# Kernel optimization log

Hardware: AMD Instinct MI355X
Metric: run time of the kernel (lower is better)

Reference implementation:

```python
import jax, jax.numpy as jnp
import numpy as np

B, N, M = 8192, 4096, 256


def setup_inputs() -> dict:
    key = jax.random.key(0)
    k_x, k_keep, k_w1, k_b1, k_w2, k_b2 = jax.random.split(key, 6)
    x = jax.random.normal(k_x, (B, N), dtype=jnp.float32)
    keep = jax.random.uniform(k_keep, (B, N)) < 0.5
    x = jnp.where(keep, x, 0.0)
    # Linear params, PyTorch-style fan-in scaling
    W1 = jax.random.normal(k_w1, (N, M), dtype=jnp.float32) / np.sqrt(N)
    b1 = jax.random.normal(k_b1, (M,), dtype=jnp.float32) * 0.01
    W2 = jax.random.normal(k_w2, (M, N), dtype=jnp.float32) / np.sqrt(M)
    b2 = jax.random.normal(k_b2, (N,), dtype=jnp.float32) * 0.01
    return {"x": x, "W1": W1, "b1": b1, "W2": W2, "b2": b2}


def reference(x, W1, b1, W2, b2):
    # f2(relu(f1(x)))
    f = jax.nn.relu(x @ W1 + b1) @ W2 + b2  # [B, N]
    mask = x != 0
    # per-row sum over masked positions (vectorized version of the Python loop)
    s = jnp.sum(jnp.where(mask, f, 0.0), axis=1, keepdims=True)  # [B, 1]
    # rows with empty mask stay all-zero; guard divide-by-zero for those rows
    s_safe = jnp.where(s == 0.0, 1.0, s)
    y = jnp.where(mask, f / s_safe, 0.0)
    return y
```

## Files before the change

### kernel.cpp

```cpp
#include <hip/hip_runtime.h>

typedef _Float16 f16;
typedef _Float16 f16x8 __attribute__((ext_vector_type(8)));
typedef float f32x4 __attribute__((ext_vector_type(4)));

#define MFMA16(a,b,c) __builtin_amdgcn_mfma_f32_16x16x32_f16((a),(b),(c),0,0,0)

__device__ __forceinline__ void gload16(const void* g, void* l) {
  __builtin_amdgcn_global_load_lds(
      (const __attribute__((address_space(1))) void*)g,
      (__attribute__((address_space(3))) void*)l, 16, 0, 0);
}

__device__ __forceinline__ int swz(int r, int c) {
  return r * 32 + ((c ^ (r & 3)) << 3);
}

__device__ __forceinline__ void split8n(const f32x4 v0, const f32x4 v1,
                                        f16x8& hv, f16x8& lv) {
#pragma unroll
  for (int j = 0; j < 4; ++j) {
    f16 h0 = (f16)v0[j]; hv[j] = h0; lv[j] = (f16)(v0[j] - (float)h0);
    f16 h1 = (f16)v1[j]; hv[j + 4] = h1; lv[j + 4] = (f16)(v1[j] - (float)h1);
  }
}

__global__ __launch_bounds__(256) void k_prep(const float* __restrict__ in,
                                              f16* __restrict__ oh, f16* __restrict__ ol,
                                              int R, int C, int trShift) {
  __shared__ float t[64][65];
  int c0 = blockIdx.x * 64, r0 = blockIdx.y * 64;
  int tid = threadIdx.x;
#pragma unroll
  for (int i = 0; i < 16; ++i) {
    int idx = tid + i * 256;
    int r = idx >> 6, c = idx & 63;
    t[r][c] = in[(size_t)(r0 + r) * C + (c0 + c)];
  }
  __syncthreads();
  int ktiles = R >> 5;
  int TRm1 = (1 << trShift) - 1;
#pragma unroll
  for (int w = 0; w < 2; ++w) {
    int idx = tid + w * 256;
    int nn = idx >> 3, cc8 = idx & 7;
    f32x4 v0, v1;
#pragma unroll
    for (int j = 0; j < 4; ++j) v0[j] = t[cc8 * 8 + j][nn];
#pragma unroll
    for (int j = 0; j < 4; ++j) v1[j] = t[cc8 * 8 + 4 + j][nn];
    f16x8 hv, lv;
    split8n(v0, v1, hv, lv);
    int gn = c0 + nn, gk = r0 + cc8 * 8;
    size_t tileIdx = (size_t)(gn >> trShift) * ktiles + (gk >> 5);
    size_t off = (tileIdx << (trShift + 5)) + ((size_t)(gn & TRm1) << 5) +
                 (((cc8 & 3) ^ (gn & 3)) << 3);
    *(f16x8*)&oh[off] = hv;
    *(f16x8*)&ol[off] = lv;
  }
}

__global__ __launch_bounds__(256, 2) void k_g1(
    const float* __restrict__ X, const f16* __restrict__ Bht,
    const f16* __restrict__ Blt, unsigned short* __restrict__ mb2,
    float* __restrict__ partials) {
  __shared__ f16 smA[2][2][4096];
  __shared__ f16 smB[2][2][4096];
  int bx = blockIdx.x, nb = blockIdx.y, kc = blockIdx.z;
  int tid = threadIdx.x;
  int wv = tid >> 6, ln = tid & 63, lr = ln & 15, lg = ln >> 4;
  int wr = wv >> 1, wc = wv & 1;
  const int NS = 32;
  int m0 = bx * 128, kb0 = kc * 1024;
  int arow = tid >> 1, akc = tid & 1;
  const float* xp = X + (size_t)(m0 + arow) * 4096 + kb0 + akc * 16;
  size_t bt0 = ((size_t)nb * 128 + (size_t)kc * 32) * 4096;
  bool domask = (nb == 0);
  int wo0 = swz(arow, 2 * akc);
  int wo1 = swz(arow, 2 * akc + 1);

  auto stageB = [&](int s, int buf) {
#pragma unroll
    for (int w = 0; w < 2; ++w) {
      size_t o = (size_t)(w * 4 + wv) * 512 + (size_t)ln * 8;
      gload16(Bht + bt0 + (size_t)s * 4096 + o, &smB[buf][0][(w * 4 + wv) * 512]);
      gload16(Blt + bt0 + (size_t)s * 4096 + o, &smB[buf][1][(w * 4 + wv) * 512]);
    }
  };
  auto commitA = [&](f32x4 a0, f32x4 a1, f32x4 a2, f32x4 a3, int buf, int s) {
    f16x8 h0, l0, h1, l1;
    split8n(a0, a1, h0, l0);
    split8n(a2, a3, h1, l1);
    *(f16x8*)&smA[buf][0][wo0] = h0;
    *(f16x8*)&smA[buf][0][wo1] = h1;
    *(f16x8*)&smA[buf][1][wo0] = l0;
    *(f16x8*)&smA[buf][1][wo1] = l1;
    if (domask) {
      unsigned m = 0;
#pragma unroll
      for (int j = 0; j < 4; ++j) {
        if (a0[j] != 0.f) m |= 1u << j;
        if (a1[j] != 0.f) m |= 1u << (4 + j);
        if (a2[j] != 0.f) m |= 1u << (8 + j);
        if (a3[j] != 0.f) m |= 1u << (12 + j);
      }
      int gk = kb0 + s * 32 + akc * 16;
      mb2[((size_t)(m0 + arow) * 512 + (gk >> 3)) >> 1] = (unsigned short)m;
    }
  };

  f32x4 acc[4][4] = {};

  stageB(0, 0);
  {
    f32x4 a0 = *(const f32x4*)xp, a1 = *(const f32x4*)(xp + 4);
    f32x4 a2 = *(const f32x4*)(xp + 8), a3 = *(const f32x4*)(xp + 12);
    commitA(a0, a1, a2, a3, 0, 0);
  }
  __syncthreads();

  int cur = 0;
  for (int s = 0; s < NS; ++s) {
    f32x4 a0, a1, a2, a3;
    bool more = (s + 1) < NS;
    if (more) {
      const float* xn = xp + (s + 1) * 32;
      a0 = *(const f32x4*)xn; a1 = *(const f32x4*)(xn + 4);
      a2 = *(const f32x4*)(xn + 8); a3 = *(const f32x4*)(xn + 12);
      stageB(s + 1, cur ^ 1);
    }
    f16x8 fah[4], fal[4], fbh[4], fbl[4];
#pragma unroll
    for (int f = 0; f < 4; ++f) {
      int r = wr * 64 + f * 16 + lr;
      fah[f] = *(const f16x8*)&smA[cur][0][swz(r, lg)];
      fal[f] = *(const f16x8*)&smA[cur][1][swz(r, lg)];
      int c = wc * 64 + f * 16 + lr;
      fbh[f] = *(const f16x8*)&smB[cur][0][swz(c, lg)];
      fbl[f] = *(const f16x8*)&smB[cur][1][swz(c, lg)];
    }
#pragma unroll
    for (int fi = 0; fi < 4; ++fi)
#pragma unroll
      for (int fj = 0; fj < 4; ++fj) {
        acc[fi][fj] = MFMA16(fah[fi], fbh[fj], acc[fi][fj]);
        acc[fi][fj] = MFMA16(fah[fi], fbl[fj], acc[fi][fj]);
        acc[fi][fj] = MFMA16(fal[fi], fbh[fj], acc[fi][fj]);
      }
    if (more) commitA(a0, a1, a2, a3, cur ^ 1, s + 1);
    __syncthreads();
    cur ^= 1;
  }

  float* pout = partials + (size_t)kc * 8192 * 256;
#pragma unroll
  for (int fi = 0; fi < 4; ++fi)
#pragma unroll
    for (int fj = 0; fj < 4; ++fj)
#pragma unroll
      for (int q = 0; q < 4; ++q) {
        int row = m0 + wr * 64 + fi * 16 + lg * 4 + q;
        int col = nb * 128 + wc * 64 + fj * 16 + lr;
        pout[(size_t)row * 256 + col] = acc[fi][fj][q];
      }
}

__global__ __launch_bounds__(256) void k_hsplit(const float* __restrict__ p,
                                                const float* __restrict__ b1,
                                                f16* __restrict__ Hh,
                                                f16* __restrict__ Hl) {
  int g = blockIdx.x * 256 + threadIdx.x;
  int r = g >> 5, c = g & 31;
  const size_t CH = (size_t)8192 * 256;
  const float* p0 = p + (size_t)r * 256 + c * 8;
  f32x4 s0 = *(const f32x4*)p0, s1 = *(const f32x4*)(p0 + 4);
#pragma unroll
  for (int q = 1; q < 4; ++q) {
    f32x4 d0 = *(const f32x4*)(p0 + q * CH), d1 = *(const f32x4*)(p0 + q * CH + 4);
#pragma unroll
    for (int j = 0; j < 4; ++j) { s0[j] += d0[j]; s1[j] += d1[j]; }
  }
  f32x4 bb0 = *(const f32x4*)(b1 + c * 8), bb1 = *(const f32x4*)(b1 + c * 8 + 4);
  f32x4 v0, v1;
#pragma unroll
  for (int j = 0; j < 4; ++j) {
    float v = s0[j] + bb0[j];
    v0[j] = v > 0.f ? v : 0.f;
    float w = s1[j] + bb1[j];
    v1[j] = w > 0.f ? w : 0.f;
  }
  f16x8 hv, lv;
  split8n(v0, v1, hv, lv);
  size_t tileIdx = (size_t)(r >> 7) * 8 + (c >> 2);
  size_t off = tileIdx * 4096 + ((size_t)(r & 127) << 5) + (((c & 3) ^ (r & 3)) << 3);
  *(f16x8*)&Hh[off] = hv;
  *(f16x8*)&Hl[off] = lv;
}

__global__ __launch_bounds__(256, 2) void k_gemm2b(
    const f16* __restrict__ At_h, const f16* __restrict__ At_l,
    const f16* __restrict__ Bt_h, const f16* __restrict__ Bt_l,
    const float* __restrict__ b2, const unsigned* __restrict__ maskw,
    f16* __restrict__ fout, float* __restrict__ partials) {
  __shared__ f16 smA[2][2][4096];
  __shared__ f16 smB[2][2][4096];
  __shared__ unsigned mlds[128][4];
  __shared__ float rsum[128][2];
  int bx = blockIdx.x, by = blockIdx.y;
  int m0 = bx * 128, n0 = by * 128;
  int tid = threadIdx.x;
  int wv = tid >> 6, ln = tid & 63, lr = ln & 15, lg = ln >> 4;
  int wr = wv >> 1, wc = wv & 1;
#pragma unroll
  for (int i = 0; i < 2; ++i) {
    int idx = tid + i * 256;
    mlds[idx >> 2][idx & 3] =
        maskw[(size_t)(m0 + (idx >> 2)) * 128 + by * 4 + (idx & 3)];
  }
  size_t at0 = (size_t)bx * 8 * 4096;
  size_t bt0 = (size_t)by * 8 * 4096;

  auto stage = [&](int s, int buf) {
#pragma unroll
    for (int w = 0; w < 2; ++w) {
      size_t o = (size_t)(w * 4 + wv) * 512 + (size_t)ln * 8;
      gload16(At_h + at0 + (size_t)s * 4096 + o, &smA[buf][0][(w * 4 + wv) * 512]);
      gload16(At_l + at0 + (size_t)s * 4096 + o, &smA[buf][1][(w * 4 + wv) * 512]);
      gload16(Bt_h + bt0 + (size_t)s * 4096 + o, &smB[buf][0][(w * 4 + wv) * 512]);
      gload16(Bt_l + bt0 + (size_t)s * 4096 + o, &smB[buf][1][(w * 4 + wv) * 512]);
    }
  };

  f32x4 acc[4][4] = {};
  stage(0, 0);
  __syncthreads();
  int cur = 0;
  for (int s = 0; s < 8; ++s) {
    if (s + 1 < 8) stage(s + 1, cur ^ 1);
    f16x8 fah[4], fal[4], fbh[4], fbl[4];
#pragma unroll
    for (int f = 0; f < 4; ++f) {
      int r = wr * 64 + f * 16 + lr;
      fah[f] = *(const f16x8*)&smA[cur][0][swz(r, lg)];
      fal[f] = *(const f16x8*)&smA[cur][1][swz(r, lg)];
      int c = wc * 64 + f * 16 + lr;
      fbh[f] = *(const f16x8*)&smB[cur][0][swz(c, lg)];
      fbl[f] = *(const f16x8*)&smB[cur][1][swz(c, lg)];
    }
#pragma unroll
    for (int fi = 0; fi < 4; ++fi)
#pragma unroll
      for (int fj = 0; fj < 4; ++fj) {
        acc[fi][fj] = MFMA16(fah[fi], fbh[fj], acc[fi][fj]);
        acc[fi][fj] = MFMA16(fah[fi], fbl[fj], acc[fi][fj]);
        acc[fi][fj] = MFMA16(fal[fi], fbh[fj], acc[fi][fj]);
      }
    __syncthreads();
    cur ^= 1;
  }

  float rp[4][4] = {};
#pragma unroll
  for (int fi = 0; fi < 4; ++fi)
#pragma unroll
    for (int fj = 0; fj < 4; ++fj)
#pragma unroll
      for (int q = 0; q < 4; ++q) {
        int row = wr * 64 + fi * 16 + lg * 4 + q;
        int col = wc * 64 + fj * 16 + lr;
        float v = acc[fi][fj][q] + b2[n0 + col];
        unsigned wd = mlds[row][col >> 5];
        float mv = ((wd >> (col & 31)) & 1u) ? v : 0.f;
        fout[(size_t)(m0 + row) * 4096 + (n0 + col)] = (f16)mv;
        rp[fi][q] += mv;
      }
#pragma unroll
  for (int fi = 0; fi < 4; ++fi)
#pragma unroll
    for (int q = 0; q < 4; ++q) {
      float sv = rp[fi][q];
      sv += __shfl_xor(sv, 1);
      sv += __shfl_xor(sv, 2);
      sv += __shfl_xor(sv, 4);
      sv += __shfl_xor(sv, 8);
      if (lr == 0) rsum[wr * 64 + fi * 16 + lg * 4 + q][wc] = sv;
    }
  __syncthreads();
  if (tid < 128)
    partials[(size_t)(m0 + tid) * 32 + by] = rsum[tid][0] + rsum[tid][1];
}

__global__ __launch_bounds__(256) void k_rowinv(const float* __restrict__ partials,
                                                float* __restrict__ inv) {
  int r = blockIdx.x * 256 + threadIdx.x;
  if (r < 8192) {
    float s = 0.f;
#pragma unroll 4
    for (int i = 0; i < 32; ++i) s += partials[(size_t)r * 32 + i];
    float ss = (s == 0.f) ? 1.f : s;
    inv[r] = 1.f / ss;
  }
}

__global__ __launch_bounds__(256) void k_scale16(const f16* __restrict__ f,
                                                 const float* __restrict__ inv,
                                                 float* __restrict__ out) {
  int v = blockIdx.x * 256 + threadIdx.x;
  float iv = inv[v >> 9];
  f16x8 d = *(const f16x8*)(f + (size_t)v * 8);
  f32x4 o0, o1;
#pragma unroll
  for (int j = 0; j < 4; ++j) {
    o0[j] = (float)d[j] * iv;
    o1[j] = (float)d[4 + j] * iv;
  }
  *(f32x4*)(out + (size_t)v * 8) = o0;
  *(f32x4*)(out + (size_t)v * 8 + 4) = o1;
}

extern "C" void kernel_launch(void* const* d_in, const int* in_sizes, int n_in,
                              void* d_out, int out_size, void* d_ws, size_t ws_size,
                              hipStream_t stream) {
  const float* x  = (const float*)d_in[0];
  const float* W1 = (const float*)d_in[1];
  const float* b1 = (const float*)d_in[2];
  const float* W2 = (const float*)d_in[3];
  const float* b2 = (const float*)d_in[4];
  float* out = (float*)d_out;
  char* ws = (char*)d_ws;

  const size_t MB = (size_t)1 << 20;
  f16* W1t_h = (f16*)(ws + 0 * MB);
  f16* W1t_l = (f16*)(ws + 2 * MB);
  f16* W2t_h = (f16*)(ws + 4 * MB);
  f16* W2t_l = (f16*)(ws + 6 * MB);
  f16* Hh    = (f16*)(ws + 8 * MB);
  f16* Hl    = (f16*)(ws + 12 * MB);
  unsigned char* mb = (unsigned char*)(ws + 16 * MB);
  float* part1 = (float*)(ws + 20 * MB);
  float* part2 = (float*)(ws + 52 * MB);
  float* inv_s = (float*)(ws + 53 * MB);
  f16* fbuf    = (f16*)(ws + 54 * MB);

  k_prep<<<dim3(4, 64), 256, 0, stream>>>(W1, W1t_h, W1t_l, 4096, 256, 7);
  k_prep<<<dim3(64, 4), 256, 0, stream>>>(W2, W2t_h, W2t_l, 256, 4096, 7);
  k_g1<<<dim3(64, 2, 4), 256, 0, stream>>>(x, W1t_h, W1t_l,
                                           (unsigned short*)mb, part1);
  k_hsplit<<<1024, 256, 0, stream>>>(part1, b1, Hh, Hl);
  k_gemm2b<<<dim3(64, 32), 256, 0, stream>>>(Hh, Hl, W2t_h, W2t_l, b2,
                                             (const unsigned*)mb, fbuf, part2);
  k_rowinv<<<32, 256, 0, stream>>>(part2, inv_s);
  k_scale16<<<16384, 256, 0, stream>>>(fbuf, inv_s, out);
}
```

Measured before the change: 215.2 us.

## Restructure first GEMM: register-resident A fragments, triple-buffered B, split-K 8

The first GEMM kernel now loads X directly into registers in MFMA fragment layout and does the fp16 hi/lo split there, so the A tile no longer goes through shared memory. Blocks shrink to 128 threads (2 waves, each covering 64 rows by all 128 columns). B tiles are triple-buffered with explicit vmcnt waits and raw s_barrier calls so the load for stage s+2 overlaps compute on stage s. Split-K goes from 4 to 8, which raises block count; in exchange the partial buffer doubles and the reduction in k_hsplit reads twice as many partials. This is meant to cut LDS traffic and barrier stalls and to improve latency hiding, at the cost of more accumulator registers and extra partial-sum memory traffic.

Measured after the change: 230.4 us. 7.1% more time.

```diff
diff --git a/kernel.cpp b/kernel.cpp
--- a/kernel.cpp
+++ b/kernel.cpp
@@ -60,107 +60,121 @@
   }
 }
 
-__global__ __launch_bounds__(256, 2) void k_g1(
+__global__ __launch_bounds__(128, 2) void k_g1(
     const float* __restrict__ X, const f16* __restrict__ Bht,
-    const f16* __restrict__ Blt, unsigned short* __restrict__ mb2,
+    const f16* __restrict__ Blt, unsigned char* __restrict__ mb,
     float* __restrict__ partials) {
-  __shared__ f16 smA[2][2][4096];
-  __shared__ f16 smB[2][2][4096];
+  __shared__ f16 smB[3][8192];
   int bx = blockIdx.x, nb = blockIdx.y, kc = blockIdx.z;
   int tid = threadIdx.x;
-  int wv = tid >> 6, ln = tid & 63, lr = ln & 15, lg = ln >> 4;
-  int wr = wv >> 1, wc = wv & 1;
-  const int NS = 32;
-  int m0 = bx * 128, kb0 = kc * 1024;
-  int arow = tid >> 1, akc = tid & 1;
-  const float* xp = X + (size_t)(m0 + arow) * 4096 + kb0 + akc * 16;
-  size_t bt0 = ((size_t)nb * 128 + (size_t)kc * 32) * 4096;
+  int wid = tid >> 6, ln = tid & 63, lr = ln & 15, lg = ln >> 4;
+  const int NS = 16;
+  int m0 = bx * 128, kb0 = kc * 512;
+  size_t bt0 = ((size_t)nb * 128 + (size_t)kc * 16) * 4096;
   bool domask = (nb == 0);
-  int wo0 = swz(arow, 2 * akc);
-  int wo1 = swz(arow, 2 * akc + 1);
-
+
+  const float* xb = X + (size_t)(m0 + wid * 64 + lr) * 4096 + kb0 + lg * 8;
+  const size_t XF = (size_t)16 * 4096;
+
+  f32x4 areg[8];
+  f16x8 ah[4], al[4];
+  f32x4 acc[4][8] = {};
+
+  auto issueA = [&](int s) {
+#pragma unroll
+    for (int fi = 0; fi < 4; ++fi) {
+      const float* p = xb + (size_t)fi * XF + s * 32;
+      areg[fi * 2] = *(const f32x4*)p;
+      areg[fi * 2 + 1] = *(const f32x4*)(p + 4);
+    }
+  };
   auto stageB = [&](int s, int buf) {
-#pragma unroll
-    for (int w = 0; w < 2; ++w) {
-      size_t o = (size_t)(w * 4 + wv) * 512 + (size_t)ln * 8;
-      gload16(Bht + bt0 + (size_t)s * 4096 + o, &smB[buf][0][(w * 4 + wv) * 512]);
-      gload16(Blt + bt0 + (size_t)s * 4096 + o, &smB[buf][1][(w * 4 + wv) * 512]);
-    }
+    const f16* bh = Bht + bt0 + (size_t)s * 4096;
+    const f16* bl = Blt + bt0 + (size_t)s * 4096;
+#pragma unroll
+    for (int i = 0; i < 4; ++i)
+      gload16(bh + ((i * 2 + wid) * 512 + ln * 8), &smB[buf][(i * 2 + wid) * 512]);
+#pragma unroll
+    for (int i = 0; i < 4; ++i)
+      gload16(bl + ((i * 2 + wid) * 512 + ln * 8),
+              &smB[buf][4096 + (i * 2 + wid) * 512]);
   };
-  auto commitA = [&](f32x4 a0, f32x4 a1, f32x4 a2, f32x4 a3, int buf, int s) {
-    f16x8 h0, l0, h1, l1;
-    split8n(a0, a1, h0, l0);
-    split8n(a2, a3, h1, l1);
-    *(f16x8*)&smA[buf][0][wo0] = h0;
-    *(f16x8*)&smA[buf][0][wo1] = h1;
-    *(f16x8*)&smA[buf][1][wo0] = l0;
-    *(f16x8*)&smA[buf][1][wo1] = l1;
+  auto splitA = [&](int s) {
+#pragma unroll
+    for (int fi = 0; fi < 4; ++fi)
+      split8n(areg[fi * 2], areg[fi * 2 + 1], ah[fi], al[fi]);
     if (domask) {
-      unsigned m = 0;
+#pragma unroll
+      for (int fi = 0; fi < 4; ++fi) {
+        unsigned m = 0;
+#pragma unroll
+        for (int j = 0; j < 4; ++j) {
+          if (areg[fi * 2][j] != 0.f) m |= 1u << j;
+          if (areg[fi * 2 + 1][j] != 0.f) m |= 1u << (4 + j);
+        }
+        int row = m0 + wid * 64 + fi * 16 + lr;
+        int gk = kb0 + s * 32 + lg * 8;
+        mb[(size_t)row * 512 + (gk >> 3)] = (unsigned char)m;
+      }
+    }
+  };
+
+  issueA(0);
+  stageB(0, 0);
+  stageB(1, 1);
+  asm volatile("s_waitcnt vmcnt(8)" ::: "memory");
+  __builtin_amdgcn_sched_barrier(0);
+  splitA(0);
+  __builtin_amdgcn_s_barrier();
+
+  int cb = 0;
+  for (int s = 0; s < NS; ++s) {
+    bool moreA = (s + 1) < NS;
+    bool moreB = (s + 2) < NS;
+    if (moreA) issueA(s + 1);
+    if (moreB) {
+      int pb = cb + 2; if (pb >= 3) pb -= 3;
+      stageB(s + 2, pb);
+    }
+#pragma unroll
+    for (int g = 0; g < 2; ++g) {
+      f16x8 fbh[4], fbl[4];
 #pragma unroll
       for (int j = 0; j < 4; ++j) {
-        if (a0[j] != 0.f) m |= 1u << j;
-        if (a1[j] != 0.f) m |= 1u << (4 + j);
-        if (a2[j] != 0.f) m |= 1u << (8 + j);
-        if (a3[j] != 0.f) m |= 1u << (12 + j);
-      }
-      int gk = kb0 + s * 32 + akc * 16;
-      mb2[((size_t)(m0 + arow) * 512 + (gk >> 3)) >> 1] = (unsigned short)m;
-    }
-  };
-
-  f32x4 acc[4][4] = {};
-
-  stageB(0, 0);
-  {
-    f32x4 a0 = *(const f32x4*)xp, a1 = *(const f32x4*)(xp + 4);
-    f32x4 a2 = *(const f32x4*)(xp + 8), a3 = *(const f32x4*)(xp + 12);
-    commitA(a0, a1, a2, a3, 0, 0);
-  }
-  __syncthreads();
-
-  int cur = 0;
-  for (int s = 0; s < NS; ++s) {
-    f32x4 a0, a1, a2, a3;
-    bool more = (s + 1) < NS;
-    if (more) {
-      const float* xn = xp + (s + 1) * 32;
-      a0 = *(const f32x4*)xn; a1 = *(const f32x4*)(xn + 4);
-      a2 = *(const f32x4*)(xn + 8); a3 = *(const f32x4*)(xn + 12);
-      stageB(s + 1, cur ^ 1);
-    }
-    f16x8 fah[4], fal[4], fbh[4], fbl[4];
-#pragma unroll
-    for (int f = 0; f < 4; ++f) {
-      int r = wr * 64 + f * 16 + lr;
-      fah[f] = *(const f16x8*)&smA[cur][0][swz(r, lg)];
-      fal[f] = *(const f16x8*)&smA[cur][1][swz(r, lg)];
-      int c = wc * 64 + f * 16 + lr;
-      fbh[f] = *(const f16x8*)&smB[cur][0][swz(c, lg)];
-      fbl[f] = *(const f16x8*)&smB[cur][1][swz(c, lg)];
-    }
-#pragma unroll
-    for (int fi = 0; fi < 4; ++fi)
-#pragma unroll
-      for (int fj = 0; fj < 4; ++fj) {
-        acc[fi][fj] = MFMA16(fah[fi], fbh[fj], acc[fi][fj]);
-        acc[fi][fj] = MFMA16(fah[fi], fbl[fj], acc[fi][fj]);
-        acc[fi][fj] = MFMA16(fal[fi], fbh[fj], acc[fi][fj]);
-      }
-    if (more) commitA(a0, a1, a2, a3, cur ^ 1, s + 1);
-    __syncthreads();
-    cur ^= 1;
+        int c = (g * 4 + j) * 16 + lr;
+        fbh[j] = *(const f16x8*)&smB[cb][swz(c, lg)];
+        fbl[j] = *(const f16x8*)&smB[cb][4096 + swz(c, lg)];
+      }
+#pragma unroll
+      for (int fi = 0; fi < 4; ++fi)
+#pragma unroll
+        for (int j = 0; j < 4; ++j) {
+          acc[fi][g * 4 + j] = MFMA16(ah[fi], fbh[j], acc[fi][g * 4 + j]);
+          acc[fi][g * 4 + j] = MFMA16(ah[fi], fbl[j], acc[fi][g * 4 + j]);
+          acc[fi][g * 4 + j] = MFMA16(al[fi], fbh[j], acc[fi][g * 4 + j]);
+        }
+    }
+    if (s + 1 < NS) {
+      if (moreB)
+        asm volatile("s_waitcnt vmcnt(8)" ::: "memory");
+      else
+        asm volatile("s_waitcnt vmcnt(0)" ::: "memory");
+      __builtin_amdgcn_sched_barrier(0);
+      splitA(s + 1);
+      __builtin_amdgcn_s_barrier();
+    }
+    cb = cb + 1; if (cb >= 3) cb -= 3;
   }
 
   float* pout = partials + (size_t)kc * 8192 * 256;
 #pragma unroll
   for (int fi = 0; fi < 4; ++fi)
 #pragma unroll
-    for (int fj = 0; fj < 4; ++fj)
+    for (int fj = 0; fj < 8; ++fj)
 #pragma unroll
       for (int q = 0; q < 4; ++q) {
-        int row = m0 + wr * 64 + fi * 16 + lg * 4 + q;
-        int col = nb * 128 + wc * 64 + fj * 16 + lr;
+        int row = m0 + wid * 64 + fi * 16 + lg * 4 + q;
+        int col = nb * 128 + fj * 16 + lr;
         pout[(size_t)row * 256 + col] = acc[fi][fj][q];
       }
 }
@@ -175,7 +189,7 @@
   const float* p0 = p + (size_t)r * 256 + c * 8;
   f32x4 s0 = *(const f32x4*)p0, s1 = *(const f32x4*)(p0 + 4);
 #pragma unroll
-  for (int q = 1; q < 4; ++q) {
+  for (int q = 1; q < 8; ++q) {
     f32x4 d0 = *(const f32x4*)(p0 + q * CH), d1 = *(const f32x4*)(p0 + q * CH + 4);
 #pragma unroll
     for (int j = 0; j < 4; ++j) { s0[j] += d0[j]; s1[j] += d1[j]; }
@@ -338,14 +352,13 @@
   f16* Hl    = (f16*)(ws + 12 * MB);
   unsigned char* mb = (unsigned char*)(ws + 16 * MB);
   float* part1 = (float*)(ws + 20 * MB);
-  float* part2 = (float*)(ws + 52 * MB);
-  float* inv_s = (float*)(ws + 53 * MB);
-  f16* fbuf    = (f16*)(ws + 54 * MB);
+  float* part2 = (float*)(ws + 84 * MB);
+  float* inv_s = (float*)(ws + 85 * MB);
+  f16* fbuf    = (f16*)(ws + 86 * MB);
 
   k_prep<<<dim3(4, 64), 256, 0, stream>>>(W1, W1t_h, W1t_l, 4096, 256, 7);
   k_prep<<<dim3(64, 4), 256, 0, stream>>>(W2, W2t_h, W2t_l, 256, 4096, 7);
-  k_g1<<<dim3(64, 2, 4), 256, 0, stream>>>(x, W1t_h, W1t_l,
-                                           (unsigned short*)mb, part1);
+  k_g1<<<dim3(64, 2, 8), 128, 0, stream>>>(x, W1t_h, W1t_l, mb, part1);
   k_hsplit<<<1024, 256, 0, stream>>>(part1, b1, Hh, Hl);
   k_gemm2b<<<dim3(64, 32), 256, 0, stream>>>(Hh, Hl, W2t_h, W2t_l, b2,
                                              (const unsigned*)mb, fbuf, part2);
```
